# Kernel optimization log

Hardware: AMD Instinct MI355X
Metric: run time of the kernel (lower is better)

Reference implementation:

```python
import jax, jax.numpy as jnp
import numpy as np
import math

D_MODEL = 1024
N_HEADS = 16
HEAD_DIM = D_MODEL // N_HEADS


def _compute_slopes(n_heads: int) -> np.ndarray:
    def pow2_slopes(n):
        start = 2.0 ** (-(2.0 ** (-(math.log2(n) - 3))))
        return [start * (start ** i) for i in range(n)]
    if math.log2(n_heads).is_integer():
        s = pow2_slopes(n_heads)
    else:
        cp = 2 ** math.floor(math.log2(n_heads))
        s = pow2_slopes(cp) + pow2_slopes(2 * cp)[0::2][: n_heads - cp]
    return np.asarray(s, dtype=np.float32)


def setup_inputs() -> dict:
    key = jax.random.key(0)
    ks = jax.random.split(key, 11)
    B, T, D = 2, 2048, D_MODEL
    scale = 1.0 / math.sqrt(D)
    inp = {
        "query": jax.random.normal(ks[0], (B, T, D), jnp.float32),
        "key": jax.random.normal(ks[1], (B, T, D), jnp.float32),
        "value": jax.random.normal(ks[2], (B, T, D), jnp.float32),
        "Wq": jax.random.normal(ks[3], (D, D), jnp.float32) * scale,
        "bq": jnp.zeros((D,), jnp.float32),
        "Wk": jax.random.normal(ks[4], (D, D), jnp.float32) * scale,
        "bk": jnp.zeros((D,), jnp.float32),
        "Wv": jax.random.normal(ks[5], (D, D), jnp.float32) * scale,
        "bv": jnp.zeros((D,), jnp.float32),
        "Wo": jax.random.normal(ks[6], (D, D), jnp.float32) * scale,
        "bo": jnp.zeros((D,), jnp.float32),
    }
    return inp


def reference(query, key, value, Wq, bq, Wk, bk, Wv, bv, Wo, bo):
    B, Tq, D = query.shape
    Tk = key.shape[1]
    H, hd = N_HEADS, HEAD_DIM
    scale = hd ** -0.5

    # projections -> [B, H, T, hd]
    Q = (query @ Wq + bq).reshape(B, Tq, H, hd).transpose(0, 2, 1, 3)
    K = (key @ Wk + bk).reshape(B, Tk, H, hd).transpose(0, 2, 1, 3)
    V = (value @ Wv + bv).reshape(B, Tk, H, hd).transpose(0, 2, 1, 3)

    # scores [B, H, Tq, Tk]
    attn = jnp.einsum("bhqd,bhkd->bhqk", Q, K) * scale

    # ALiBi bias (only applied when Tq == Tk, mirroring the original)
    slopes = jnp.asarray(_compute_slopes(H))  # [H]
    pos = jnp.arange(Tq)
    dist = -jnp.abs(pos[None, :] - pos[:, None]).astype(jnp.float32)  # [Tq, Tk]
    bias = slopes[:, None, None] * dist[None]  # [H, Tq, Tk]
    attn = attn + bias[None]

    attn = jax.nn.softmax(attn, axis=-1)
    out = jnp.einsum("bhqk,bhkd->bhqd", attn, V)
    out = out.transpose(0, 2, 1, 3).reshape(B, Tq, D)
    return out @ Wo + bo
```

## Files before the change

kernel.cpp:

```cpp
#include <hip/hip_runtime.h>
#include <stdint.h>

#define BSZ 2
#define TT 2048
#define DD 1024
#define HH 16
#define HD 64

typedef __bf16 bf16x8 __attribute__((ext_vector_type(8)));
typedef float f32x4 __attribute__((ext_vector_type(4)));

#if __has_builtin(__builtin_amdgcn_exp2f)
__device__ __forceinline__ float fexp2(float x) { return __builtin_amdgcn_exp2f(x); }
#else
__device__ __forceinline__ float fexp2(float x) {
    float r; asm("v_exp_f32 %0, %1\n\ts_nop 1" : "=v"(r) : "v"(x)); return r;
}
#endif

__device__ __forceinline__ unsigned short f2bf(float f) {
    union { float f; unsigned u; } c; c.f = f;
    unsigned u = c.u;
    unsigned r = u + 0x7fffu + ((u >> 16) & 1u);
    return (unsigned short)(r >> 16);
}
__device__ __forceinline__ unsigned fasu(float f) {
    union { float f; unsigned u; } c; c.f = f; return c.u;
}

union U4BF { uint4 u; bf16x8 b; };
__device__ __forceinline__ bf16x8 as_bf8(uint4 v) { U4BF c; c.u = v; return c.b; }

#if __has_builtin(__builtin_amdgcn_global_load_lds)
__device__ __forceinline__ void gl_lds16(const ushort* g, ushort* l) {
    __builtin_amdgcn_global_load_lds(
        (const __attribute__((address_space(1))) uint32_t*)g,
        (__attribute__((address_space(3))) uint32_t*)l, 16, 0, 0);
}
#define GLL_LANE 1
#else
__device__ __forceinline__ void gl_lds16_fallback(const ushort* g, ushort* l, int lane) {
    *(uint4*)(l + lane * 8) = *(const uint4*)(g);
}
#define GLL_LANE 0
#endif

__global__ __launch_bounds__(256)
void prep(const float* __restrict__ q, const float* __restrict__ k,
          const float* __restrict__ v,
          const float* __restrict__ W0, const float* __restrict__ W1,
          const float* __restrict__ W2, const float* __restrict__ W3,
          ushort* __restrict__ xq, ushort* __restrict__ xk, ushort* __restrict__ xv,
          ushort* __restrict__ T0, ushort* __restrict__ T1,
          ushort* __restrict__ T2, ushort* __restrict__ T3,
          int* __restrict__ ctr) {
    __shared__ float sh[32][33];
    const int y = blockIdx.y;
    if (y < 3) {
        const float* in = (y == 0) ? q : (y == 1) ? k : v;
        ushort* out = (y == 0) ? xq : (y == 1) ? xk : xv;
        int i = blockIdx.x * 256 + threadIdx.x;
        float4 val = ((const float4*)in)[i];
        ushort4 o;
        o.x = f2bf(val.x); o.y = f2bf(val.y); o.z = f2bf(val.z); o.w = f2bf(val.w);
        ((ushort4*)out)[i] = o;
    } else {
        if (blockIdx.x == 0 && threadIdx.x == 0) *ctr = 1024;
        const int x = blockIdx.x;
        const float* src; ushort* dst;
        switch (x >> 10) {
            case 0:  src = W0; dst = T0; break;
            case 1:  src = W1; dst = T1; break;
            case 2:  src = W2; dst = T2; break;
            default: src = W3; dst = T3; break;
        }
        const int tile = x & 1023;
        const int k0 = (tile >> 5) * 32, n0 = (tile & 31) * 32;
        const int tx = threadIdx.x & 31, ty = threadIdx.x >> 5;
        #pragma unroll
        for (int p = 0; p < 4; ++p)
            sh[ty + 8 * p][tx] = src[(size_t)(k0 + ty + 8 * p) * DD + n0 + tx];
        __syncthreads();
        #pragma unroll
        for (int p = 0; p < 4; ++p)
            dst[(size_t)(n0 + ty + 8 * p) * DD + k0 + tx] = f2bf(sh[tx][ty + 8 * p]);
    }
}

template<int BM, int OUT_MODE>
__global__ __launch_bounds__(256)
void gemm_mfma(const ushort* __restrict__ A0, const ushort* __restrict__ B0,
               const float* __restrict__ c0, void* __restrict__ d0,
               const ushort* __restrict__ A1, const ushort* __restrict__ B1,
               const float* __restrict__ c1, void* __restrict__ d1,
               const ushort* __restrict__ A2, const ushort* __restrict__ B2,
               const float* __restrict__ c2, void* __restrict__ d2) {
    constexpr int TI = 4;
    constexpr int TJ = (BM == 128) ? 4 : 2;
    constexpr int WC = (BM == 128) ? 2 : 4;
    __shared__ __attribute__((aligned(16))) ushort As[BM][32];
    __shared__ __attribute__((aligned(16))) ushort Bs[128][32];
    const ushort* A; const ushort* Bt; const float* bias; void* outp;
    const int z = blockIdx.z;
    switch (z) {
        case 0:  A = A0; Bt = B0; bias = c0; outp = d0; break;
        case 1:  A = A1; Bt = B1; bias = c1; outp = d1; break;
        default: A = A2; Bt = B2; bias = c2; outp = d2; break;
    }
    const int tid  = threadIdx.x;
    const int lane = tid & 63, w = tid >> 6;
    const int wr = w / WC, wc = w % WC;
    const int ln = lane & 15, quad = lane >> 4;
    const int m0 = blockIdx.y * BM, n0 = blockIdx.x * 128;

    const f32x4 zero = {0.f, 0.f, 0.f, 0.f};
    f32x4 acc[TI][TJ];
    #pragma unroll
    for (int i = 0; i < TI; ++i)
        #pragma unroll
        for (int j = 0; j < TJ; ++j) acc[i][j] = zero;

    const int lr  = lane >> 2;
    const int lc8 = (lane & 3) * 8;

    for (int kb = 0; kb < 1024; kb += 32) {
        #pragma unroll
        for (int it = 0; it < BM / 64; ++it) {
            int r0 = it * 64 + w * 16;
#if GLL_LANE
            gl_lds16(A + (size_t)(m0 + r0 + lr) * 1024 + kb + lc8, &As[r0][0]);
#else
            gl_lds16_fallback(A + (size_t)(m0 + r0 + lr) * 1024 + kb + lc8, &As[r0][0], lane);
#endif
        }
        #pragma unroll
        for (int it = 0; it < 2; ++it) {
            int r0 = it * 64 + w * 16;
#if GLL_LANE
            gl_lds16(Bt + (size_t)(n0 + r0 + lr) * 1024 + kb + lc8, &Bs[r0][0]);
#else
            gl_lds16_fallback(Bt + (size_t)(n0 + r0 + lr) * 1024 + kb + lc8, &Bs[r0][0], lane);
#endif
        }
        __syncthreads();
        bf16x8 af[TI], bfr[TJ];
        #pragma unroll
        for (int i = 0; i < TI; ++i)
            af[i] = as_bf8(*(const uint4*)&As[wr * 64 + i * 16 + ln][quad * 8]);
        #pragma unroll
        for (int j = 0; j < TJ; ++j)
            bfr[j] = as_bf8(*(const uint4*)&Bs[wc * (TJ * 16) + j * 16 + ln][quad * 8]);
        #pragma unroll
        for (int i = 0; i < TI; ++i)
            #pragma unroll
            for (int j = 0; j < TJ; ++j)
                acc[i][j] = __builtin_amdgcn_mfma_f32_16x16x32_bf16(af[i], bfr[j], acc[i][j], 0, 0, 0);
        __syncthreads();
    }

    #pragma unroll
    for (int j = 0; j < TJ; ++j) {
        int n = n0 + wc * (TJ * 16) + j * 16 + ln;
        float bv = bias[n];
        #pragma unroll
        for (int i = 0; i < TI; ++i) {
            int mb = m0 + wr * 64 + i * 16 + quad * 4;
            if (OUT_MODE == 0 && z == 2) {
                int b = mb >> 11, t = mb & 2047, h = n >> 6, d = n & 63;
                ushort4 pk;
                pk.x = f2bf(acc[i][j][0] + bv);
                pk.y = f2bf(acc[i][j][1] + bv);
                pk.z = f2bf(acc[i][j][2] + bv);
                pk.w = f2bf(acc[i][j][3] + bv);
                *(ushort4*)((ushort*)outp + ((size_t)((b * HH + h) * HD + d)) * TT + t) = pk;
            } else {
                #pragma unroll
                for (int r = 0; r < 4; ++r) {
                    int m = mb + r;
                    float v = acc[i][j][r] + bv;
                    if (OUT_MODE == 0) {
                        int b = m >> 11, t = m & 2047, h = n >> 6, d = n & 63;
                        ((ushort*)outp)[(((size_t)(b * HH + h)) * TT + t) * HD + d] = f2bf(v);
                    } else {
                        ((float*)outp)[(size_t)m * 1024 + n] = v;
                    }
                }
            }
        }
    }
}

__global__ __launch_bounds__(256)
void attn_kernel(const ushort* __restrict__ Qh, const ushort* __restrict__ Kh,
                 const ushort* __restrict__ Vtg, ushort* __restrict__ outp,
                 int* __restrict__ ctr) {
    __shared__ __attribute__((aligned(16))) char smem[33792];
    __shared__ int s_item;
    ushort (*Ps)[32][72] = (ushort (*)[32][72])smem;
    float  (*Rbuf)[64][44] = (float (*)[64][44])smem;

    const int tid  = threadIdx.x;
    const int lane = tid & 63, w = tid >> 6;
    const int ln = lane & 15, quad = lane >> 4;

    bf16x8 ones;
    {
        union { ushort us[8]; bf16x8 v; } uu;
        #pragma unroll
        for (int p = 0; p < 8; ++p) uu.us[p] = 0x3F80;
        ones = uu.v;
    }
    const f32x4 zero = {0.f, 0.f, 0.f, 0.f};
    const float c1 = 0.125f * 1.44269504f;

    int item = ((blockIdx.x & 7) << 7) | (blockIdx.x >> 3);
    while (item < 2048) {
        const int h = 15 - (item >> 7);
        const int rr = item & 127;
        const int b = rr & 1;
        const int qt = rr >> 1;
        const int bh = b * 16 + h;
        const int qbase = qt * 32;
        const float slope2 = exp2f(-0.5f * (float)(h + 1)) * 1.44269504f;
        const size_t base = (size_t)bh * (TT * HD);

        const int D = (int)ceilf(18.0f / slope2);
        int lo = qbase - D;
        int kt_lo = (lo > 0) ? (lo >> 6) : 0;
        int kt_hi = (qbase + 32 + D + 63) >> 6;
        if (kt_hi > TT / 64) kt_hi = TT / 64;
        const int nt = kt_hi - kt_lo;
        const int cs = (nt + 3) >> 2;
        const int my_lo = kt_lo + w * cs;
        const int my_hi = (my_lo + cs < kt_hi) ? (my_lo + cs) : kt_hi;

        bf16x8 qa[2][2];
        #pragma unroll
        for (int g = 0; g < 2; ++g) {
            const uint4* qp = (const uint4*)(Qh + base + (size_t)(qbase + g * 16 + ln) * HD);
            qa[g][0] = as_bf8(qp[quad]);
            qa[g][1] = as_bf8(qp[4 + quad]);
        }
        f32x4 o[2][4], lsum[2];
        #pragma unroll
        for (int g = 0; g < 2; ++g) {
            lsum[g] = zero;
            #pragma unroll
            for (int dn = 0; dn < 4; ++dn) o[g][dn] = zero;
        }
        float qrf[2][4];
        #pragma unroll
        for (int g = 0; g < 2; ++g)
            #pragma unroll
            for (int r = 0; r < 4; ++r)
                qrf[g][r] = (float)(qbase + g * 16 + quad * 4 + r);

        const ushort* kp = Kh  + base + (size_t)ln * HD + quad * 8;
        const ushort* vp = Vtg + base + (size_t)ln * TT + quad * 8;

        if (my_lo < my_hi) {
            uint4 kf[8];
            {
                const int ko = my_lo * 4096;
                #pragma unroll
                for (int n = 0; n < 4; ++n)
                    #pragma unroll
                    for (int hf = 0; hf < 2; ++hf)
                        kf[n * 2 + hf] = *(const uint4*)(kp + ko + n * 1024 + hf * 32);
            }

            for (int kt = my_lo; kt < my_hi; ++kt) {
                uint4 vf[8];
                {
                    const int vo = kt * 64;
                    #pragma unroll
                    for (int dn = 0; dn < 4; ++dn)
                        #pragma unroll
                        for (int hf = 0; hf < 2; ++hf)
                            vf[dn * 2 + hf] = *(const uint4*)(vp + dn * 32768 + vo + hf * 32);
                }
                uint4 kn[8];
                if (kt + 1 < my_hi) {
                    const int ko = (kt + 1) * 4096;
                    #pragma unroll
                    for (int n = 0; n < 4; ++n)
                        #pragma unroll
                        for (int hf = 0; hf < 2; ++hf)
                            kn[n * 2 + hf] = *(const uint4*)(kp + ko + n * 1024 + hf * 32);
                }

                f32x4 s[2][4];
                #pragma unroll
                for (int n = 0; n < 4; ++n) {
                    bf16x8 b0 = as_bf8(kf[n * 2]);
                    bf16x8 b1 = as_bf8(kf[n * 2 + 1]);
                    #pragma unroll
                    for (int g = 0; g < 2; ++g) {
                        f32x4 zz = zero;
                        zz = __builtin_amdgcn_mfma_f32_16x16x32_bf16(qa[g][0], b0, zz, 0, 0, 0);
                        s[g][n] = __builtin_amdgcn_mfma_f32_16x16x32_bf16(qa[g][1], b1, zz, 0, 0, 0);
                    }
                }

                #pragma unroll
                for (int n = 0; n < 4; ++n) {
                    float kg = (float)(kt * 64 + n * 16 + ln);
                    int bswz = ((2 * n + (ln >> 3)) ^ quad) * 8 + (ln & 7);
                    #pragma unroll
                    for (int g = 0; g < 2; ++g) {
                        #pragma unroll
                        for (int r = 0; r < 4; ++r) {
                            float d = qrf[g][r] - kg;
                            float arg = fmaf(s[g][n][r], c1, -slope2 * fabsf(d));
                            float p = fexp2(arg);
                            Ps[w][g * 16 + quad * 4 + r][bswz] = (ushort)(fasu(p) >> 16);
                        }
                    }
                }

                #pragma unroll
                for (int hf = 0; hf < 2; ++hf) {
                    bf16x8 ap0 = as_bf8(*(const uint4*)&Ps[w][ln]     [((hf * 4 + quad) ^ (ln >> 2)) * 8]);
                    bf16x8 ap1 = as_bf8(*(const uint4*)&Ps[w][16 + ln][((hf * 4 + quad) ^ (ln >> 2)) * 8]);
                    #pragma unroll
                    for (int dn = 0; dn < 4; ++dn) {
                        bf16x8 bv = as_bf8(vf[dn * 2 + hf]);
                        o[0][dn] = __builtin_amdgcn_mfma_f32_16x16x32_bf16(ap0, bv, o[0][dn], 0, 0, 0);
                        o[1][dn] = __builtin_amdgcn_mfma_f32_16x16x32_bf16(ap1, bv, o[1][dn], 0, 0, 0);
                    }
                    lsum[0] = __builtin_amdgcn_mfma_f32_16x16x32_bf16(ap0, ones, lsum[0], 0, 0, 0);
                    lsum[1] = __builtin_amdgcn_mfma_f32_16x16x32_bf16(ap1, ones, lsum[1], 0, 0, 0);
                }

                #pragma unroll
                for (int i = 0; i < 8; ++i) kf[i] = kn[i];
            }
        }

        __syncthreads();
        if (w > 0) {
            float* dst = &Rbuf[w - 1][lane][0];
            #pragma unroll
            for (int g = 0; g < 2; ++g) {
                #pragma unroll
                for (int dn = 0; dn < 4; ++dn)
                    #pragma unroll
                    for (int r = 0; r < 4; ++r)
                        dst[g * 16 + dn * 4 + r] = o[g][dn][r];
                #pragma unroll
                for (int r = 0; r < 4; ++r)
                    dst[32 + g * 4 + r] = lsum[g][r];
            }
        }
        __syncthreads();
        if (w == 0) {
            #pragma unroll
            for (int j = 0; j < 3; ++j) {
                const float* src = &Rbuf[j][lane][0];
                #pragma unroll
                for (int g = 0; g < 2; ++g) {
                    #pragma unroll
                    for (int dn = 0; dn < 4; ++dn)
                        #pragma unroll
                        for (int r = 0; r < 4; ++r)
                            o[g][dn][r] += src[g * 16 + dn * 4 + r];
                    #pragma unroll
                    for (int r = 0; r < 4; ++r)
                        lsum[g][r] += src[32 + g * 4 + r];
                }
            }
            #pragma unroll
            for (int g = 0; g < 2; ++g) {
                #pragma unroll
                for (int r = 0; r < 4; ++r) {
                    float inv = __builtin_amdgcn_rcpf(lsum[g][r]);
                    int q = qbase + g * 16 + quad * 4 + r;
                    size_t ob = ((size_t)(b * TT + q)) * DD + h * HD;
                    #pragma unroll
                    for (int dn = 0; dn < 4; ++dn)
                        outp[ob + dn * 16 + ln] = f2bf(o[g][dn][r] * inv);
                }
            }
        }

        __syncthreads();
        if (tid == 0) s_item = atomicAdd(ctr, 1);
        __syncthreads();
        item = s_item;
    }
}

extern "C" void kernel_launch(void* const* d_in, const int* in_sizes, int n_in,
                              void* d_out, int out_size, void* d_ws, size_t ws_size,
                              hipStream_t stream) {
    const float* query = (const float*)d_in[0];
    const float* key   = (const float*)d_in[1];
    const float* value = (const float*)d_in[2];
    const float* Wq = (const float*)d_in[3];
    const float* bq = (const float*)d_in[4];
    const float* Wk = (const float*)d_in[5];
    const float* bk = (const float*)d_in[6];
    const float* Wv = (const float*)d_in[7];
    const float* bv = (const float*)d_in[8];
    const float* Wo = (const float*)d_in[9];
    const float* bo = (const float*)d_in[10];
    float* out = (float*)d_out;

    char* ws = (char*)d_ws;
    const size_t MB = 1024 * 1024;
    ushort* Xq  = (ushort*)(ws + 0);
    ushort* Xk  = (ushort*)(ws + 8 * MB);
    ushort* Xv  = (ushort*)(ws + 16 * MB);
    ushort* Wtq = (ushort*)(ws + 24 * MB);
    ushort* Wtk = (ushort*)(ws + 26 * MB);
    ushort* Wtv = (ushort*)(ws + 28 * MB);
    ushort* Wto = (ushort*)(ws + 30 * MB);
    ushort* Qh  = (ushort*)(ws + 32 * MB);
    ushort* Kh  = (ushort*)(ws + 40 * MB);
    ushort* Vt  = (ushort*)(ws + 48 * MB);
    ushort* attn = (ushort*)(ws + 0);
    int* ctr = (int*)d_out;

    prep<<<dim3(4096, 4), 256, 0, stream>>>(query, key, value, Wq, Wk, Wv, Wo,
                                            Xq, Xk, Xv, Wtq, Wtk, Wtv, Wto, ctr);

    gemm_mfma<128, 0><<<dim3(8, 32, 3), 256, 0, stream>>>(
        Xq, Wtq, bq, Qh,  Xk, Wtk, bk, Kh,  Xv, Wtv, bv, Vt);

    attn_kernel<<<dim3(1024), 256, 0, stream>>>(Qh, Kh, Vt, attn, ctr);

    gemm_mfma<64, 1><<<dim3(8, 64, 1), 256, 0, stream>>>(
        attn, Wto, bo, out,  attn, Wto, bo, out,  attn, Wto, bo, out);
}
```

Measured before the change: 248.0 us.

## Share double-buffered K/V tiles in LDS across waves handling different query tiles

The attention kernel now gives each block 128 query rows, one 32-row tile per wave, instead of splitting one 32-row tile's key range across 4 waves. K and V tiles are staged cooperatively into swizzled, double-buffered shared memory with global-to-LDS loads and read by all waves. This removes the cross-wave reduction and the atomic work-queue loop, and launches a fixed 512-block grid. The aim is to cut redundant global K/V loads through reuse. In exchange, waves sit idle on tiles outside their own ALiBi window and pay a block barrier every key tile.

```diff
diff --git a/kernel.cpp b/kernel.cpp
--- a/kernel.cpp
+++ b/kernel.cpp
@@ -52,8 +52,7 @@
           const float* __restrict__ W2, const float* __restrict__ W3,
           ushort* __restrict__ xq, ushort* __restrict__ xk, ushort* __restrict__ xv,
           ushort* __restrict__ T0, ushort* __restrict__ T1,
-          ushort* __restrict__ T2, ushort* __restrict__ T3,
-          int* __restrict__ ctr) {
+          ushort* __restrict__ T2, ushort* __restrict__ T3) {
     __shared__ float sh[32][33];
     const int y = blockIdx.y;
     if (y < 3) {
@@ -65,7 +64,6 @@
         o.x = f2bf(val.x); o.y = f2bf(val.y); o.z = f2bf(val.z); o.w = f2bf(val.w);
         ((ushort4*)out)[i] = o;
     } else {
-        if (blockIdx.x == 0 && threadIdx.x == 0) *ctr = 1024;
         const int x = blockIdx.x;
         const float* src; ushort* dst;
         switch (x >> 10) {
@@ -192,16 +190,19 @@
 
 __global__ __launch_bounds__(256)
 void attn_kernel(const ushort* __restrict__ Qh, const ushort* __restrict__ Kh,
-                 const ushort* __restrict__ Vtg, ushort* __restrict__ outp,
-                 int* __restrict__ ctr) {
-    __shared__ __attribute__((aligned(16))) char smem[33792];
-    __shared__ int s_item;
-    ushort (*Ps)[32][72] = (ushort (*)[32][72])smem;
-    float  (*Rbuf)[64][44] = (float (*)[64][44])smem;
+                 const ushort* __restrict__ Vtg, ushort* __restrict__ outp) {
+    __shared__ __attribute__((aligned(16))) ushort Ks[2][64][64];
+    __shared__ __attribute__((aligned(16))) ushort Vs[2][64][64];
+    __shared__ __attribute__((aligned(16))) ushort Ps[4][32][72];
 
     const int tid  = threadIdx.x;
     const int lane = tid & 63, w = tid >> 6;
     const int ln = lane & 15, quad = lane >> 4;
+    const int rr = lane >> 3, jj = lane & 7;
+    const int sswz = (jj ^ rr) * 8;
+    const int l7 = ln & 7;
+    const int u0 = (quad ^ l7) * 8;
+    const int u1 = u0 ^ 32;
 
     bf16x8 ones;
     {
@@ -213,180 +214,129 @@
     const f32x4 zero = {0.f, 0.f, 0.f, 0.f};
     const float c1 = 0.125f * 1.44269504f;
 
-    int item = ((blockIdx.x & 7) << 7) | (blockIdx.x >> 3);
-    while (item < 2048) {
-        const int h = 15 - (item >> 7);
-        const int rr = item & 127;
-        const int b = rr & 1;
-        const int qt = rr >> 1;
-        const int bh = b * 16 + h;
-        const int qbase = qt * 32;
-        const float slope2 = exp2f(-0.5f * (float)(h + 1)) * 1.44269504f;
-        const size_t base = (size_t)bh * (TT * HD);
-
-        const int D = (int)ceilf(18.0f / slope2);
-        int lo = qbase - D;
-        int kt_lo = (lo > 0) ? (lo >> 6) : 0;
-        int kt_hi = (qbase + 32 + D + 63) >> 6;
-        if (kt_hi > TT / 64) kt_hi = TT / 64;
-        const int nt = kt_hi - kt_lo;
-        const int cs = (nt + 3) >> 2;
-        const int my_lo = kt_lo + w * cs;
-        const int my_hi = (my_lo + cs < kt_hi) ? (my_lo + cs) : kt_hi;
-
-        bf16x8 qa[2][2];
-        #pragma unroll
-        for (int g = 0; g < 2; ++g) {
-            const uint4* qp = (const uint4*)(Qh + base + (size_t)(qbase + g * 16 + ln) * HD);
-            qa[g][0] = as_bf8(qp[quad]);
-            qa[g][1] = as_bf8(qp[4 + quad]);
-        }
-        f32x4 o[2][4], lsum[2];
-        #pragma unroll
-        for (int g = 0; g < 2; ++g) {
-            lsum[g] = zero;
-            #pragma unroll
-            for (int dn = 0; dn < 4; ++dn) o[g][dn] = zero;
-        }
-        float qrf[2][4];
-        #pragma unroll
-        for (int g = 0; g < 2; ++g)
-            #pragma unroll
-            for (int r = 0; r < 4; ++r)
-                qrf[g][r] = (float)(qbase + g * 16 + quad * 4 + r);
-
-        const ushort* kp = Kh  + base + (size_t)ln * HD + quad * 8;
-        const ushort* vp = Vtg + base + (size_t)ln * TT + quad * 8;
-
-        if (my_lo < my_hi) {
-            uint4 kf[8];
-            {
-                const int ko = my_lo * 4096;
+    const int item = blockIdx.x;
+    const int h = 15 - (item >> 5);
+    const int sub = item & 31;
+    const int b = sub & 1;
+    const int qt = sub >> 1;
+    const int bh = b * 16 + h;
+    const int qb0 = qt * 128;
+    const int qbw = qb0 + w * 32;
+    const float slope2 = exp2f(-0.5f * (float)(h + 1)) * 1.44269504f;
+    const size_t base = (size_t)bh * (TT * HD);
+
+    const int D = (int)ceilf(18.0f / slope2);
+    int lo = qb0 - D;
+    int kt_lo = (lo > 0) ? (lo >> 6) : 0;
+    int kt_hi = (qb0 + 128 + D + 63) >> 6;
+    if (kt_hi > TT / 64) kt_hi = TT / 64;
+    int wl = qbw - D;
+    int my_lo = (wl > 0) ? (wl >> 6) : 0;
+    if (my_lo < kt_lo) my_lo = kt_lo;
+    int my_hi = (qbw + 32 + D + 63) >> 6;
+    if (my_hi > kt_hi) my_hi = kt_hi;
+
+    bf16x8 qa[2][2];
+    #pragma unroll
+    for (int g = 0; g < 2; ++g) {
+        const uint4* qp = (const uint4*)(Qh + base + (size_t)(qbw + g * 16 + ln) * HD);
+        qa[g][0] = as_bf8(qp[quad]);
+        qa[g][1] = as_bf8(qp[4 + quad]);
+    }
+    f32x4 o[2][4], lsum[2];
+    #pragma unroll
+    for (int g = 0; g < 2; ++g) {
+        lsum[g] = zero;
+        #pragma unroll
+        for (int dn = 0; dn < 4; ++dn) o[g][dn] = zero;
+    }
+    float qrf[2][4];
+    #pragma unroll
+    for (int g = 0; g < 2; ++g)
+        #pragma unroll
+        for (int r = 0; r < 4; ++r)
+            qrf[g][r] = (float)(qbw + g * 16 + quad * 4 + r);
+
+    auto STAGE = [&](int bufi, int kt) {
+        #pragma unroll
+        for (int ii = 0; ii < 2; ++ii) {
+            const int r0 = (w * 2 + ii) * 8;
+#if GLL_LANE
+            gl_lds16(Kh + base + (size_t)(kt * 64 + r0 + rr) * HD + sswz, &Ks[bufi][r0][0]);
+            gl_lds16(Vtg + base + (size_t)(r0 + rr) * TT + kt * 64 + sswz, &Vs[bufi][r0][0]);
+#else
+            gl_lds16_fallback(Kh + base + (size_t)(kt * 64 + r0 + rr) * HD + sswz, &Ks[bufi][r0][0], lane);
+            gl_lds16_fallback(Vtg + base + (size_t)(r0 + rr) * TT + kt * 64 + sswz, &Vs[bufi][r0][0], lane);
+#endif
+        }
+    };
+
+    STAGE(0, kt_lo);
+    int buf = 0;
+    for (int kt = kt_lo; kt < kt_hi; ++kt) {
+        asm volatile("s_waitcnt vmcnt(0)" ::: "memory");
+        __syncthreads();
+        if (kt + 1 < kt_hi) STAGE(buf ^ 1, kt + 1);
+
+        if (kt >= my_lo && kt < my_hi) {
+            f32x4 s[2][4];
+            #pragma unroll
+            for (int n = 0; n < 4; ++n) {
+                bf16x8 b0 = as_bf8(*(const uint4*)&Ks[buf][n * 16 + ln][u0]);
+                bf16x8 b1 = as_bf8(*(const uint4*)&Ks[buf][n * 16 + ln][u1]);
                 #pragma unroll
-                for (int n = 0; n < 4; ++n)
-                    #pragma unroll
-                    for (int hf = 0; hf < 2; ++hf)
-                        kf[n * 2 + hf] = *(const uint4*)(kp + ko + n * 1024 + hf * 32);
+                for (int g = 0; g < 2; ++g) {
+                    f32x4 zz = zero;
+                    zz = __builtin_amdgcn_mfma_f32_16x16x32_bf16(qa[g][0], b0, zz, 0, 0, 0);
+                    s[g][n] = __builtin_amdgcn_mfma_f32_16x16x32_bf16(qa[g][1], b1, zz, 0, 0, 0);
+                }
             }
 
-            for (int kt = my_lo; kt < my_hi; ++kt) {
-                uint4 vf[8];
-                {
-                    const int vo = kt * 64;
-                    #pragma unroll
-                    for (int dn = 0; dn < 4; ++dn)
-                        #pragma unroll
-                        for (int hf = 0; hf < 2; ++hf)
-                            vf[dn * 2 + hf] = *(const uint4*)(vp + dn * 32768 + vo + hf * 32);
-                }
-                uint4 kn[8];
-                if (kt + 1 < my_hi) {
-                    const int ko = (kt + 1) * 4096;
-                    #pragma unroll
-                    for (int n = 0; n < 4; ++n)
-                        #pragma unroll
-                        for (int hf = 0; hf < 2; ++hf)
-                            kn[n * 2 + hf] = *(const uint4*)(kp + ko + n * 1024 + hf * 32);
-                }
-
-                f32x4 s[2][4];
-                #pragma unroll
-                for (int n = 0; n < 4; ++n) {
-                    bf16x8 b0 = as_bf8(kf[n * 2]);
-                    bf16x8 b1 = as_bf8(kf[n * 2 + 1]);
-                    #pragma unroll
-                    for (int g = 0; g < 2; ++g) {
-                        f32x4 zz = zero;
-                        zz = __builtin_amdgcn_mfma_f32_16x16x32_bf16(qa[g][0], b0, zz, 0, 0, 0);
-                        s[g][n] = __builtin_amdgcn_mfma_f32_16x16x32_bf16(qa[g][1], b1, zz, 0, 0, 0);
-                    }
-                }
-
-                #pragma unroll
-                for (int n = 0; n < 4; ++n) {
-                    float kg = (float)(kt * 64 + n * 16 + ln);
-                    int bswz = ((2 * n + (ln >> 3)) ^ quad) * 8 + (ln & 7);
-                    #pragma unroll
-                    for (int g = 0; g < 2; ++g) {
-                        #pragma unroll
-                        for (int r = 0; r < 4; ++r) {
-                            float d = qrf[g][r] - kg;
-                            float arg = fmaf(s[g][n][r], c1, -slope2 * fabsf(d));
-                            float p = fexp2(arg);
-                            Ps[w][g * 16 + quad * 4 + r][bswz] = (ushort)(fasu(p) >> 16);
-                        }
-                    }
-                }
-
-                #pragma unroll
-                for (int hf = 0; hf < 2; ++hf) {
-                    bf16x8 ap0 = as_bf8(*(const uint4*)&Ps[w][ln]     [((hf * 4 + quad) ^ (ln >> 2)) * 8]);
-                    bf16x8 ap1 = as_bf8(*(const uint4*)&Ps[w][16 + ln][((hf * 4 + quad) ^ (ln >> 2)) * 8]);
-                    #pragma unroll
-                    for (int dn = 0; dn < 4; ++dn) {
-                        bf16x8 bv = as_bf8(vf[dn * 2 + hf]);
-                        o[0][dn] = __builtin_amdgcn_mfma_f32_16x16x32_bf16(ap0, bv, o[0][dn], 0, 0, 0);
-                        o[1][dn] = __builtin_amdgcn_mfma_f32_16x16x32_bf16(ap1, bv, o[1][dn], 0, 0, 0);
-                    }
-                    lsum[0] = __builtin_amdgcn_mfma_f32_16x16x32_bf16(ap0, ones, lsum[0], 0, 0, 0);
-                    lsum[1] = __builtin_amdgcn_mfma_f32_16x16x32_bf16(ap1, ones, lsum[1], 0, 0, 0);
-                }
-
-                #pragma unroll
-                for (int i = 0; i < 8; ++i) kf[i] = kn[i];
-            }
-        }
-
-        __syncthreads();
-        if (w > 0) {
-            float* dst = &Rbuf[w - 1][lane][0];
-            #pragma unroll
-            for (int g = 0; g < 2; ++g) {
-                #pragma unroll
-                for (int dn = 0; dn < 4; ++dn)
-                    #pragma unroll
-                    for (int r = 0; r < 4; ++r)
-                        dst[g * 16 + dn * 4 + r] = o[g][dn][r];
-                #pragma unroll
-                for (int r = 0; r < 4; ++r)
-                    dst[32 + g * 4 + r] = lsum[g][r];
-            }
-        }
-        __syncthreads();
-        if (w == 0) {
-            #pragma unroll
-            for (int j = 0; j < 3; ++j) {
-                const float* src = &Rbuf[j][lane][0];
+            #pragma unroll
+            for (int n = 0; n < 4; ++n) {
+                float kg = (float)(kt * 64 + n * 16 + ln);
+                int bswz = ((2 * n + (ln >> 3)) ^ quad) * 8 + (ln & 7);
                 #pragma unroll
                 for (int g = 0; g < 2; ++g) {
                     #pragma unroll
-                    for (int dn = 0; dn < 4; ++dn)
-                        #pragma unroll
-                        for (int r = 0; r < 4; ++r)
-                            o[g][dn][r] += src[g * 16 + dn * 4 + r];
-                    #pragma unroll
-                    for (int r = 0; r < 4; ++r)
-                        lsum[g][r] += src[32 + g * 4 + r];
+                    for (int r = 0; r < 4; ++r) {
+                        float d = qrf[g][r] - kg;
+                        float arg = fmaf(s[g][n][r], c1, -slope2 * fabsf(d));
+                        float p = fexp2(arg);
+                        Ps[w][g * 16 + quad * 4 + r][bswz] = (ushort)(fasu(p) >> 16);
+                    }
                 }
             }
-            #pragma unroll
-            for (int g = 0; g < 2; ++g) {
+
+            #pragma unroll
+            for (int hf = 0; hf < 2; ++hf) {
+                bf16x8 ap0 = as_bf8(*(const uint4*)&Ps[w][ln]     [((hf * 4 + quad) ^ (ln >> 2)) * 8]);
+                bf16x8 ap1 = as_bf8(*(const uint4*)&Ps[w][16 + ln][((hf * 4 + quad) ^ (ln >> 2)) * 8]);
+                const int uu = hf ? u1 : u0;
                 #pragma unroll
-                for (int r = 0; r < 4; ++r) {
-                    float inv = __builtin_amdgcn_rcpf(lsum[g][r]);
-                    int q = qbase + g * 16 + quad * 4 + r;
-                    size_t ob = ((size_t)(b * TT + q)) * DD + h * HD;
-                    #pragma unroll
-                    for (int dn = 0; dn < 4; ++dn)
-                        outp[ob + dn * 16 + ln] = f2bf(o[g][dn][r] * inv);
+                for (int dn = 0; dn < 4; ++dn) {
+                    bf16x8 bv = as_bf8(*(const uint4*)&Vs[buf][dn * 16 + ln][uu]);
+                    o[0][dn] = __builtin_amdgcn_mfma_f32_16x16x32_bf16(ap0, bv, o[0][dn], 0, 0, 0);
+                    o[1][dn] = __builtin_amdgcn_mfma_f32_16x16x32_bf16(ap1, bv, o[1][dn], 0, 0, 0);
                 }
+                lsum[0] = __builtin_amdgcn_mfma_f32_16x16x32_bf16(ap0, ones, lsum[0], 0, 0, 0);
+                lsum[1] = __builtin_amdgcn_mfma_f32_16x16x32_bf16(ap1, ones, lsum[1], 0, 0, 0);
             }
         }
-
-        __syncthreads();
-        if (tid == 0) s_item = atomicAdd(ctr, 1);
-        __syncthreads();
-        item = s_item;
+        buf ^= 1;
+    }
+
+    #pragma unroll
+    for (int g = 0; g < 2; ++g) {
+        #pragma unroll
+        for (int r = 0; r < 4; ++r) {
+            float inv = __builtin_amdgcn_rcpf(lsum[g][r]);
+            int q = qbw + g * 16 + quad * 4 + r;
+            size_t ob = ((size_t)(b * TT + q)) * DD + h * HD;
+            #pragma unroll
+            for (int dn = 0; dn < 4; ++dn)
+                outp[ob + dn * 16 + ln] = f2bf(o[g][dn][r] * inv);
+        }
     }
 }
 
@@ -419,15 +369,14 @@
     ushort* Kh  = (ushort*)(ws + 40 * MB);
     ushort* Vt  = (ushort*)(ws + 48 * MB);
     ushort* attn = (ushort*)(ws + 0);
-    int* ctr = (int*)d_out;
 
     prep<<<dim3(4096, 4), 256, 0, stream>>>(query, key, value, Wq, Wk, Wv, Wo,
-                                            Xq, Xk, Xv, Wtq, Wtk, Wtv, Wto, ctr);
+                                            Xq, Xk, Xv, Wtq, Wtk, Wtv, Wto);
 
     gemm_mfma<128, 0><<<dim3(8, 32, 3), 256, 0, stream>>>(
         Xq, Wtq, bq, Qh,  Xk, Wtk, bk, Kh,  Xv, Wtv, bv, Vt);
 
-    attn_kernel<<<dim3(1024), 256, 0, stream>>>(Qh, Kh, Vt, attn, ctr);
+    attn_kernel<<<dim3(512), 256, 0, stream>>>(Qh, Kh, Vt, attn);
 
     gemm_mfma<64, 1><<<dim3(8, 64, 1), 256, 0, stream>>>(
         attn, Wto, bo, out,  attn, Wto, bo, out,  attn, Wto, bo, out);
```

After: 228.8 us. -7.8%, faster.
